# Optimization experiments

Hardware: AMD Instinct MI355X
Metric: run time of the kernel (lower is better)

Reference implementation:

```python
import jax, jax.numpy as jnp
import numpy as np

B, T, N_STOCKS = 256, 250, 500
HIDDEN, N_LAYERS = 512, 2
LB, UB = 0.0, 0.1
N_ITER = 30  # rebalance fixed-point iterations; extra iters are exact no-ops once converged


def setup_inputs() -> dict:
    key = jax.random.key(0)
    ks = jax.random.split(key, 16)
    s = 1.0 / np.sqrt(HIDDEN)  # torch GRU init scale
    inp = {"x": jax.random.normal(ks[0], (B, T, N_STOCKS), jnp.float32)}
    in_dims = [N_STOCKS, HIDDEN]
    for l in range(N_LAYERS):
        inp[f"w_ih_l{l}"] = jax.random.uniform(ks[1 + 4 * l], (3 * HIDDEN, in_dims[l]), jnp.float32, -s, s)
        inp[f"w_hh_l{l}"] = jax.random.uniform(ks[2 + 4 * l], (3 * HIDDEN, HIDDEN), jnp.float32, -s, s)
        inp[f"b_ih_l{l}"] = jax.random.uniform(ks[3 + 4 * l], (3 * HIDDEN,), jnp.float32, -s, s)
        inp[f"b_hh_l{l}"] = jax.random.uniform(ks[4 + 4 * l], (3 * HIDDEN,), jnp.float32, -s, s)
    inp["fc_w"] = jax.random.uniform(ks[9], (N_STOCKS, HIDDEN), jnp.float32, -s, s)
    inp["fc_b"] = jax.random.uniform(ks[10], (N_STOCKS,), jnp.float32, -s, s)
    return inp


def gru_layer(x, w_ih, w_hh, b_ih, b_hh):
    # x: [B, T, D] -> hidden sequence [B, T, H]; torch gate order: r, z, n
    gi = jnp.einsum('btd,gd->btg', x, w_ih) + b_ih  # precompute input gates [B, T, 3H]

    def cell(h, gi_t):
        gh = h @ w_hh.T + b_hh
        i_r, i_z, i_n = jnp.split(gi_t, 3, axis=-1)
        h_r, h_z, h_n = jnp.split(gh, 3, axis=-1)
        r = jax.nn.sigmoid(i_r + h_r)
        z = jax.nn.sigmoid(i_z + h_z)
        n = jnp.tanh(i_n + r * h_n)
        h_new = (1.0 - z) * n + z * h
        return h_new, h_new

    h0 = jnp.zeros((x.shape[0], HIDDEN), x.dtype)
    _, hs = jax.lax.scan(cell, h0, jnp.swapaxes(gi, 0, 1))  # scan over time
    return jnp.swapaxes(hs, 0, 1)


def rebalance(w):
    # Batched capped-simplex redistribution: clamp to [LB, UB], then push the
    # clipped mass onto non-capped entries proportionally; repeat to fixed point.
    def body(w, _):
        wc = jnp.clip(w, LB, UB)
        leftover = jnp.sum(w - wc, axis=-1, keepdims=True)
        nom = jnp.where(wc != UB, wc, 0.0)
        w_new = wc + leftover * nom / jnp.sum(nom, axis=-1, keepdims=True)
        return w_new, None

    w, _ = jax.lax.scan(body, w, None, length=N_ITER)
    return w


def reference(x, w_ih_l0, w_hh_l0, b_ih_l0, b_hh_l0,
              w_ih_l1, w_hh_l1, b_ih_l1, b_hh_l1, fc_w, fc_b):
    h = gru_layer(x, w_ih_l0, w_hh_l0, b_ih_l0, b_hh_l0)
    h = gru_layer(h, w_ih_l1, w_hh_l1, b_ih_l1, b_hh_l1)
    h_t = h[:, -1, :]                      # last timestep [B, H]
    logit = h_t @ fc_w.T + fc_b            # dropout is identity at inference
    logit = jax.nn.silu(logit)             # swish
    w = jax.nn.softmax(logit, axis=-1)
    return rebalance(w)
```

## Files before the change

kernel.cpp:

```cpp
#include <hip/hip_runtime.h>
#include <math.h>

typedef __attribute__((ext_vector_type(8))) short short8;
typedef __attribute__((ext_vector_type(4))) float floatx4;
typedef unsigned short ushort_t;
typedef unsigned int uint32;
typedef unsigned long long u64;

#define BB 256
#define TT 250
#define NS 500
#define HH 512
#define NBLK 256
#define TBLK 256
#define PL_USH 131072u
#define CH_USH 8192u
#define WHI_USH 32768
#define SMEMB 131072

__device__ __forceinline__ ushort_t f2bf(float f) {
    uint32 u = __float_as_uint(f);
    u += 0x7fffu + ((u >> 16) & 1u);
    return (ushort_t)(u >> 16);
}
__device__ __forceinline__ float bf2f(ushort_t h) { return __uint_as_float(((uint32)h) << 16); }
__device__ __forceinline__ float sigm(float x) { return 1.f / (1.f + expf(-x)); }
__device__ __forceinline__ floatx4 mfma16(short8 a, short8 b, floatx4 c) {
    return __builtin_amdgcn_mfma_f32_16x16x32_bf16(a, b, c, 0, 0, 0);
}
__device__ __forceinline__ u64 pack4(const ushort_t* a) {
    return (u64)a[0] | ((u64)a[1] << 16) | ((u64)a[2] << 32) | ((u64)a[3] << 48);
}
__device__ __forceinline__ void st_agent_u32(ushort_t* p, uint32 v) {
    __hip_atomic_store((uint32*)p, v, __ATOMIC_RELAXED, __HIP_MEMORY_SCOPE_AGENT);
}
__device__ __forceinline__ void st_agent_u64(ushort_t* p, u64 v) {
    __hip_atomic_store((u64*)p, v, __ATOMIC_RELAXED, __HIP_MEMORY_SCOPE_AGENT);
}

__device__ __forceinline__ void dbar(unsigned* flags, unsigned phase, int bid) {
    __syncthreads();
    if (threadIdx.x == 0)
        __hip_atomic_store(flags + ((size_t)bid << 4), phase,
                           __ATOMIC_RELAXED, __HIP_MEMORY_SCOPE_AGENT);
    unsigned* sp = flags + ((size_t)threadIdx.x << 4);
    while (__hip_atomic_load(sp, __ATOMIC_RELAXED, __HIP_MEMORY_SCOPE_AGENT) < phase)
        __builtin_amdgcn_s_sleep(2);
    __syncthreads();
}

__device__ __forceinline__ float block_max4(float v, float* scr) {
#pragma unroll
    for (int off = 32; off; off >>= 1) v = fmaxf(v, __shfl_down(v, off, 64));
    if ((threadIdx.x & 63) == 0) scr[threadIdx.x >> 6] = v;
    __syncthreads();
    if (threadIdx.x == 0)
        scr[8] = fmaxf(fmaxf(scr[0], scr[1]), fmaxf(scr[2], scr[3]));
    __syncthreads();
    float r = scr[8];
    __syncthreads();
    return r;
}
__device__ __forceinline__ float2 block_sum2_4(float a, float b, float* scr) {
#pragma unroll
    for (int off = 32; off; off >>= 1) {
        a += __shfl_down(a, off, 64);
        b += __shfl_down(b, off, 64);
    }
    if ((threadIdx.x & 63) == 0) { int w = threadIdx.x >> 6; scr[w] = a; scr[4 + w] = b; }
    __syncthreads();
    if (threadIdx.x == 0) {
        scr[8] = scr[0] + scr[1] + scr[2] + scr[3];
        scr[9] = scr[4] + scr[5] + scr[6] + scr[7];
    }
    __syncthreads();
    float2 r = make_float2(scr[8], scr[9]);
    __syncthreads();
    return r;
}

__device__ __forceinline__ void gemm_both(const ushort_t* __restrict__ gp,
                                          const ushort_t* __restrict__ hp,
                                          const ushort_t* whiS, const ushort_t* wloS,
                                          floatx4 (&aGI)[2][2], floatx4 (&aGH)[2][2]) {
    short8 Bh0[12], Bh1[12], Bl0[12], Bl1[12];
    const ushort_t* gpl = gp + PL_USH;
    const ushort_t* hpl = hp + PL_USH;

#define ISSUE(pc) do {                                                                    \
        const ushort_t* _ph = ((pc) < 16) ? (gp + (size_t)(pc) * CH_USH)                  \
                                          : (hp + (size_t)((pc) - 16) * CH_USH);          \
        const ushort_t* _pl = ((pc) < 16) ? (gpl + (size_t)(pc) * CH_USH)                 \
                                          : (hpl + (size_t)((pc) - 16) * CH_USH);         \
        asm volatile("global_load_dwordx4 %0, %1, off sc0 sc1"                            \
                     : "=v"(Bh0[(pc) % 12]) : "v"(_ph));                                  \
        asm volatile("global_load_dwordx4 %0, %1, off offset:1024 sc0 sc1"                \
                     : "=v"(Bh1[(pc) % 12]) : "v"(_ph));                                  \
        asm volatile("global_load_dwordx4 %0, %1, off sc0 sc1"                            \
                     : "=v"(Bl0[(pc) % 12]) : "v"(_pl));                                  \
        asm volatile("global_load_dwordx4 %0, %1, off offset:1024 sc0 sc1"                \
                     : "=v"(Bl1[(pc) % 12]) : "v"(_pl));                                  \
    } while (0)

    ISSUE(0); ISSUE(1); ISSUE(2); ISSUE(3); ISSUE(4); ISSUE(5);
    ISSUE(6); ISSUE(7); ISSUE(8); ISSUE(9); ISSUE(10);

    short8 w0h = *(const short8*)(whiS);
    short8 w1h = *(const short8*)(whiS + 512);
    short8 w0l = *(const short8*)(wloS);
    short8 w1l = *(const short8*)(wloS + 512);

#define GSTEP(c, N) do {                                                                  \
        if ((c) + 11 < 32) ISSUE((c) + 11);                                               \
        short8 n0h, n1h, n0l, n1l;                                                        \
        if ((c) + 1 < 32) {                                                               \
            const size_t _w = (size_t)(((c) + 1) * 2) * 512;                              \
            n0h = *(const short8*)(whiS + _w);                                            \
            n1h = *(const short8*)(whiS + _w + 512);                                      \
            n0l = *(const short8*)(wloS + _w);                                            \
            n1l = *(const short8*)(wloS + _w + 512);                                      \
        }                                                                                 \
        asm volatile("s_waitcnt vmcnt(" #N ")" ::: "memory");                             \
        __builtin_amdgcn_sched_barrier(0);                                                \
        const int _cs = (c) % 12;                                                         \
        floatx4 (&A)[2][2] = ((c) < 16) ? aGI : aGH;                                      \
        A[0][0] = mfma16(w0h, Bh0[_cs], A[0][0]);                                         \
        A[0][1] = mfma16(w0h, Bh1[_cs], A[0][1]);                                         \
        A[1][0] = mfma16(w1h, Bh0[_cs], A[1][0]);                                         \
        A[1][1] = mfma16(w1h, Bh1[_cs], A[1][1]);                                         \
        A[0][0] = mfma16(w0h, Bl0[_cs], A[0][0]);                                         \
        A[0][1] = mfma16(w0h, Bl1[_cs], A[0][1]);                                         \
        A[1][0] = mfma16(w1h, Bl0[_cs], A[1][0]);                                         \
        A[1][1] = mfma16(w1h, Bl1[_cs], A[1][1]);                                         \
        A[0][0] = mfma16(w0l, Bh0[_cs], A[0][0]);                                         \
        A[0][1] = mfma16(w0l, Bh1[_cs], A[0][1]);                                         \
        A[1][0] = mfma16(w1l, Bh0[_cs], A[1][0]);                                         \
        A[1][1] = mfma16(w1l, Bh1[_cs], A[1][1]);                                         \
        if ((c) + 1 < 32) { w0h = n0h; w1h = n1h; w0l = n0l; w1l = n1l; }                 \
    } while (0)

    GSTEP(0, 44);  GSTEP(1, 44);  GSTEP(2, 44);  GSTEP(3, 44);  GSTEP(4, 44);
    GSTEP(5, 44);  GSTEP(6, 44);  GSTEP(7, 44);  GSTEP(8, 44);  GSTEP(9, 44);
    GSTEP(10, 44); GSTEP(11, 44); GSTEP(12, 44); GSTEP(13, 44); GSTEP(14, 44);
    GSTEP(15, 44); GSTEP(16, 44); GSTEP(17, 44); GSTEP(18, 44); GSTEP(19, 44);
    GSTEP(20, 44); GSTEP(21, 40); GSTEP(22, 36); GSTEP(23, 32); GSTEP(24, 28);
    GSTEP(25, 24); GSTEP(26, 20); GSTEP(27, 16); GSTEP(28, 12); GSTEP(29, 8);
    GSTEP(30, 4);  GSTEP(31, 0);
#undef GSTEP
#undef ISSUE
}

__global__ void __launch_bounds__(TBLK, 1)
gru_main(const float* __restrict__ x,
         const float* __restrict__ wih0, const float* __restrict__ whh0,
         const float* __restrict__ bi0,  const float* __restrict__ bh0,
         const float* __restrict__ wih1, const float* __restrict__ whh1,
         const float* __restrict__ bi1,  const float* __restrict__ bh1,
         const float* __restrict__ fcb,  const float* __restrict__ fcT,
         ushort_t* xpack, ushort_t* h0pack, ushort_t* h1pack,
         unsigned* flags,
         float* __restrict__ out)
{
    extern __shared__ char smem_raw[];
    ushort_t* whi = (ushort_t*)smem_raw;
    ushort_t* wlo = whi + WHI_USH;

    const int bid = blockIdx.x, tid = threadIdx.x;
    const int L  = bid >> 7;
    const int UG = (bid >> 1) & 63;
    const int CT = bid & 1;
    const int wid = tid >> 6, lane = tid & 63;

    {
        const float* Wgi = L ? wih1 : wih0;
        const float* Wgh = L ? whh1 : whh0;
        const int Kgi = L ? HH : NS;
        for (int idx = tid; idx < 32768; idx += TBLK) {
            const int j = idx & 7, ln = (idx >> 3) & 63, rc = idx >> 9;
            const int c = rc >> 1, rt = rc & 1;
            const int m = ln & 15, qq = ln >> 4;
            const int lr = rt * 16 + m;
            const int g = lr >> 3, u = lr & 7;
            float v = 0.f;
            if (g < 3) {
                if (c < 16) {
                    const int k = c * 32 + qq * 8 + j;
                    if (k < Kgi) v = Wgi[(size_t)(g * HH + UG * 8 + u) * Kgi + k];
                } else {
                    const int k = (c - 16) * 32 + qq * 8 + j;
                    v = Wgh[(size_t)(g * HH + UG * 8 + u) * HH + k];
                }
            }
            const ushort_t hb = f2bf(v);
            whi[idx] = hb;
            wlo[idx] = f2bf(v - bf2f(hb));
        }
    }

    const int ub = ((lane >> 4) & 1) * 4;
    float biR[4], biZ[4], biN[4], bhR[4], bhZ[4], bhN[4];
    {
        const float* bi = L ? bi1 : bi0;
        const float* bh = L ? bh1 : bh0;
#pragma unroll
        for (int p = 0; p < 4; ++p) {
            const int ugl = UG * 8 + ub + p;
            biR[p] = bi[ugl]; biZ[p] = bi[HH + ugl]; biN[p] = bi[2 * HH + ugl];
            bhR[p] = bh[ugl]; bhZ[p] = bh[HH + ugl]; bhN[p] = bh[2 * HH + ugl];
        }
    }
    float hreg[2][4] = {{0.f, 0.f, 0.f, 0.f}, {0.f, 0.f, 0.f, 0.f}};
    const int chW = UG >> 2, qqW = UG & 3;
    __syncthreads();

    const ushort_t* whiS = whi + (size_t)lane * 8;
    const ushort_t* wloS = wlo + (size_t)lane * 8;
    const size_t apoff = ((size_t)(CT * 8 + wid * 2) * 64 + lane) * 8;

    unsigned phase = 0;
    for (int s = 0; s <= TT; ++s) {
        const bool active = L ? (s >= 1) : (s < TT);
        if (active) {
            const ushort_t *gisrc, *ghsrc;
            if (L == 0) {
                gisrc = xpack + (size_t)(s & 1) * 2 * PL_USH;
                ghsrc = h0pack + (size_t)((s - 1) & 1) * 2 * PL_USH;
            } else {
                gisrc = h0pack + (size_t)((s - 1) & 1) * 2 * PL_USH;
                ghsrc = h1pack + (size_t)(s & 1) * 2 * PL_USH;
            }
            floatx4 z4 = {0.f, 0.f, 0.f, 0.f};
            floatx4 aGI[2][2], aGH[2][2];
#pragma unroll
            for (int i = 0; i < 2; ++i) { aGI[i][0] = z4; aGI[i][1] = z4; aGH[i][0] = z4; aGH[i][1] = z4; }
            gemm_both(gisrc + apoff, ghsrc + apoff, whiS, wloS, aGI, aGH);

            float4 xv0, xv1;
            const bool doX = (s <= TT - 2) && (bid * TBLK + tid < 16384);
            int xko = 0, xb = 0;
            if (doX) {
                const int gx = bid * TBLK + tid;
                xko = gx & 63; xb = gx >> 6;
                const float* xs = x + ((size_t)xb * TT + (s + 1)) * NS + xko * 8;
                if (xko < 62) { xv0 = *(const float4*)(xs); xv1 = *(const float4*)(xs + 4); }
                else {
                    float tmp[8];
#pragma unroll
                    for (int j = 0; j < 8; ++j) {
                        const int k = xko * 8 + j;
                        tmp[j] = (k < NS) ? xs[j] : 0.f;
                    }
                    xv0 = make_float4(tmp[0], tmp[1], tmp[2], tmp[3]);
                    xv1 = make_float4(tmp[4], tmp[5], tmp[6], tmp[7]);
                }
            }

            float zGI[2][4], zGH[2][4];
#pragma unroll
            for (int t = 0; t < 2; ++t)
#pragma unroll
                for (int r = 0; r < 4; ++r) {
                    zGI[t][r] = __shfl_xor(aGI[0][t][r], 32, 64);
                    zGH[t][r] = __shfl_xor(aGH[0][t][r], 32, 64);
                }
            ushort_t* pk = L ? h1pack + (size_t)((s - 1) & 1) * 2 * PL_USH
                             : h0pack + (size_t)(s & 1) * 2 * PL_USH;
            if (lane < 32) {
#pragma unroll
                for (int t = 0; t < 2; ++t) {
                    ushort_t hi4[4], lo4[4];
#pragma unroll
                    for (int r = 0; r < 4; ++r) {
                        const float gir = aGI[0][t][r], ghr = aGH[0][t][r];
                        const float giz = zGI[t][r],    ghz = zGH[t][r];
                        const float gin = aGI[1][t][r], ghn = aGH[1][t][r];
                        const float rr = sigm(gir + biR[r] + ghr + bhR[r]);
                        const float zz = sigm(giz + biZ[r] + ghz + bhZ[r]);
                        const float nn = tanhf(gin + biN[r] + rr * (ghn + bhN[r]));
                        const float hv = (1.f - zz) * nn + zz * hreg[t][r];
                        hreg[t][r] = hv;
                        hi4[r] = f2bf(hv);
                        lo4[r] = f2bf(hv - bf2f(hi4[r]));
                    }
                    const int b = CT * 128 + wid * 32 + t * 16 + (lane & 15);
                    const size_t o8 = ((size_t)(chW * 16 + (b >> 4)) * 64 + qqW * 16 + (b & 15)) * 8 + ub;
                    st_agent_u32(pk + o8,     (uint32)hi4[0] | ((uint32)hi4[1] << 16));
                    st_agent_u32(pk + o8 + 2, (uint32)hi4[2] | ((uint32)hi4[3] << 16));
                    st_agent_u32(pk + PL_USH + o8,     (uint32)lo4[0] | ((uint32)lo4[1] << 16));
                    st_agent_u32(pk + PL_USH + o8 + 2, (uint32)lo4[2] | ((uint32)lo4[3] << 16));
                }
            }

            if (doX) {
                ushort_t hi8[8], lo8[8];
                float vv[8] = {xv0.x, xv0.y, xv0.z, xv0.w, xv1.x, xv1.y, xv1.z, xv1.w};
#pragma unroll
                for (int j = 0; j < 8; ++j) {
                    hi8[j] = f2bf(vv[j]);
                    lo8[j] = f2bf(vv[j] - bf2f(hi8[j]));
                }
                ushort_t* xp = xpack + (size_t)((s + 1) & 1) * 2 * PL_USH;
                const size_t o = ((size_t)((xko >> 2) * 16 + (xb >> 4)) * 64 + (xko & 3) * 16 + (xb & 15)) * 8;
                st_agent_u64(xp + o, pack4(hi8));
                st_agent_u64(xp + o + 4, pack4(hi8 + 4));
                st_agent_u64(xp + PL_USH + o, pack4(lo8));
                st_agent_u64(xp + PL_USH + o + 4, pack4(lo8 + 4));
            }
        } else if ((s <= TT - 2) && (bid * TBLK + tid < 16384)) {
            const int gx = bid * TBLK + tid;
            const int xko = gx & 63, xb = gx >> 6;
            const float* xs = x + ((size_t)xb * TT + (s + 1)) * NS + xko * 8;
            ushort_t hi8[8], lo8[8];
#pragma unroll
            for (int j = 0; j < 8; ++j) {
                const int k = xko * 8 + j;
                const float v = (k < NS) ? xs[j] : 0.f;
                hi8[j] = f2bf(v);
                lo8[j] = f2bf(v - bf2f(hi8[j]));
            }
            ushort_t* xp = xpack + (size_t)((s + 1) & 1) * 2 * PL_USH;
            const size_t o = ((size_t)((xko >> 2) * 16 + (xb >> 4)) * 64 + (xko & 3) * 16 + (xb & 15)) * 8;
            st_agent_u64(xp + o, pack4(hi8));
            st_agent_u64(xp + o + 4, pack4(hi8 + 4));
            st_agent_u64(xp + PL_USH + o, pack4(lo8));
            st_agent_u64(xp + PL_USH + o + 4, pack4(lo8 + 4));
        }
        ++phase;
        dbar(flags, phase, bid);
    }

    {
        const int b = bid;
        float* sh = (float*)smem_raw;
        float* scr = sh + 576;
        const ushort_t* pk = h1pack + (size_t)1 * 2 * PL_USH;
        for (int u = tid; u < HH; u += TBLK) {
            const int uo = u >> 3, j = u & 7;
            const size_t o = ((size_t)((uo >> 2) * 16 + (b >> 4)) * 64 + (uo & 3) * 16 + (b & 15)) * 8 + j;
            sh[u] = bf2f(pk[o]) + bf2f(pk[PL_USH + o]);
        }
        __syncthreads();

        const int o1 = tid;
        const bool v2 = (tid + 256) < NS;
        const int o2 = v2 ? (tid + 256) : (NS - 1);
        float a0 = fcb[o1], a1 = fcb[o2];
        for (int k = 0; k < HH; ++k) {
            const float hv = sh[k];
            const float* fr = fcT + (size_t)k * NS;
            a0 = fmaf(hv, fr[o1], a0);
            a1 = fmaf(hv, fr[o2], a1);
        }
        float l0 = a0 * sigm(a0);
        float l1 = a1 * sigm(a1);
        float mx = block_max4(fmaxf(l0, v2 ? l1 : -3.4e38f), scr);
        float e0 = expf(l0 - mx);
        float e1 = v2 ? expf(l1 - mx) : 0.f;
        float2 s2 = block_sum2_4(e0 + e1, 0.f, scr);
        float w0 = e0 / s2.x, w1 = e1 / s2.x;
        for (int it = 0; it < 30; ++it) {
            float c0v = fminf(fmaxf(w0, 0.f), 0.1f);
            float c1v = fminf(fmaxf(w1, 0.f), 0.1f);
            float lv = (w0 - c0v) + (w1 - c1v);
            float n0 = (c0v != 0.1f) ? c0v : 0.f;
            float n1 = (v2 && c1v != 0.1f) ? c1v : 0.f;
            float2 rs = block_sum2_4(lv, n0 + n1, scr);
            float inv = rs.x / rs.y;
            w0 = c0v + inv * n0;
            w1 = c1v + inv * n1;
        }
        out[(size_t)b * NS + o1] = w0;
        if (v2) out[(size_t)b * NS + tid + 256] = w1;
    }
}

__global__ void pack_x0(const float* __restrict__ x, ushort_t* __restrict__ xpack) {
    const int t = blockIdx.x * 256 + threadIdx.x;
    const int ko = t & 63, b = t >> 6;
    const float* xs = x + (size_t)b * TT * NS;
    ushort_t hi8[8], lo8[8];
#pragma unroll
    for (int j = 0; j < 8; ++j) {
        const int k = ko * 8 + j;
        const float v = (k < NS) ? xs[k] : 0.f;
        hi8[j] = f2bf(v);
        lo8[j] = f2bf(v - bf2f(hi8[j]));
    }
    const size_t o = ((size_t)((ko >> 2) * 16 + (b >> 4)) * 64 + (ko & 3) * 16 + (b & 15)) * 8;
    *(uint4*)(xpack + o) = *(uint4*)hi8;
    *(uint4*)(xpack + PL_USH + o) = *(uint4*)lo8;
}

__global__ void transpose_k(const float* __restrict__ src, float* __restrict__ dst,
                            int G, int K) {
    int idx = blockIdx.x * 256 + threadIdx.x;
    if (idx >= G * K) return;
    int k = idx / G, g = idx - k * G;
    dst[idx] = src[(size_t)g * K + k];
}

extern "C" void kernel_launch(void* const* d_in, const int* in_sizes, int n_in,
                              void* d_out, int out_size, void* d_ws, size_t ws_size,
                              hipStream_t stream) {
    const float* x    = (const float*)d_in[0];
    const float* wih0 = (const float*)d_in[1];
    const float* whh0 = (const float*)d_in[2];
    const float* bih0 = (const float*)d_in[3];
    const float* bhh0 = (const float*)d_in[4];
    const float* wih1 = (const float*)d_in[5];
    const float* whh1 = (const float*)d_in[6];
    const float* bih1 = (const float*)d_in[7];
    const float* bhh1 = (const float*)d_in[8];
    const float* fcw  = (const float*)d_in[9];
    const float* fcb  = (const float*)d_in[10];
    float* outp = (float*)d_out;

    char* ws = (char*)d_ws;
    unsigned* flags  = (unsigned*)ws;
    ushort_t* h0pack = (ushort_t*)(ws + 196608);
    ushort_t* h1pack = (ushort_t*)(ws + 196608 + 1048576);
    ushort_t* xpack  = (ushort_t*)(ws + 196608 + 2097152);
    float*    fcT    = (float*)(ws + 196608 + 3145728);

    hipMemsetAsync(ws, 0, 196608 + 2097152, stream);
    pack_x0<<<64, 256, 0, stream>>>(x, xpack);
    {
        int nel = NS * HH;
        transpose_k<<<(nel + 255) / 256, 256, 0, stream>>>(fcw, fcT, NS, HH);
    }

    hipFuncSetAttribute((const void*)gru_main,
                        hipFuncAttributeMaxDynamicSharedMemorySize, SMEMB);

    void* args[] = {(void*)&x,
                    (void*)&wih0, (void*)&whh0, (void*)&bih0, (void*)&bhh0,
                    (void*)&wih1, (void*)&whh1, (void*)&bih1, (void*)&bhh1,
                    (void*)&fcb, (void*)&fcT,
                    (void*)&xpack, (void*)&h0pack, (void*)&h1pack,
                    (void*)&flags, (void*)&outp};
    hipError_t e = hipLaunchCooperativeKernel((const void*)gru_main, dim3(NBLK), dim3(TBLK),
                                              args, SMEMB, stream);
    if (e != hipSuccess) {
        gru_main<<<dim3(NBLK), dim3(TBLK), SMEMB, stream>>>(
            x, wih0, whh0, bih0, bhh0, wih1, whh1, bih1, bhh1,
            fcb, fcT, xpack, h0pack, h1pack, flags, outp);
    }
}
```

Measured before the change: 3.342 ms.

## Use hierarchical per-XCD grid barrier with explicit fences instead of coherent stores

Replaces the flat all-blocks grid barrier with a two-level barrier. Each XCD elects a leader block that waits for its members, issues a release fence, and exchanges completion flags with the other XCD leaders before an acquire fence. Member blocks then poll a single per-XCD flag. Because the fences now provide visibility, hidden-state and x stores become plain wide stores, and the GEMM loads drop the sc1 bit. The intent is to cut polling traffic and per-store coherence cost on every timestep. The risk is memory-ordering bugs, since correctness now depends on the fences covering L2 writeback and invalidation across XCDs.

Measured after the change: 5.774 ms. 1.73x slower.

```diff
diff --git a/kernel.cpp b/kernel.cpp
--- a/kernel.cpp
+++ b/kernel.cpp
@@ -31,22 +31,56 @@
 __device__ __forceinline__ u64 pack4(const ushort_t* a) {
     return (u64)a[0] | ((u64)a[1] << 16) | ((u64)a[2] << 32) | ((u64)a[3] << 48);
 }
-__device__ __forceinline__ void st_agent_u32(ushort_t* p, uint32 v) {
-    __hip_atomic_store((uint32*)p, v, __ATOMIC_RELAXED, __HIP_MEMORY_SCOPE_AGENT);
-}
-__device__ __forceinline__ void st_agent_u64(ushort_t* p, u64 v) {
-    __hip_atomic_store((u64*)p, v, __ATOMIC_RELAXED, __HIP_MEMORY_SCOPE_AGENT);
-}
-
-__device__ __forceinline__ void dbar(unsigned* flags, unsigned phase, int bid) {
-    __syncthreads();
-    if (threadIdx.x == 0)
-        __hip_atomic_store(flags + ((size_t)bid << 4), phase,
-                           __ATOMIC_RELAXED, __HIP_MEMORY_SCOPE_AGENT);
+__device__ __forceinline__ void st_flag(unsigned* p, unsigned v) {
+    __hip_atomic_store(p, v, __ATOMIC_RELAXED, __HIP_MEMORY_SCOPE_AGENT);
+}
+__device__ __forceinline__ unsigned ld_flag(const unsigned* p) {
+    return __hip_atomic_load(p, __ATOMIC_RELAXED, __HIP_MEMORY_SCOPE_AGENT);
+}
+
+
+__device__ __forceinline__ void dbar_flat(unsigned* flags, unsigned phase, int bid) {
+    __syncthreads();
+    if (threadIdx.x == 0) st_flag(flags + ((size_t)bid << 4), phase);
     unsigned* sp = flags + ((size_t)threadIdx.x << 4);
-    while (__hip_atomic_load(sp, __ATOMIC_RELAXED, __HIP_MEMORY_SCOPE_AGENT) < phase)
-        __builtin_amdgcn_s_sleep(2);
-    __syncthreads();
+    while (ld_flag(sp) < phase) __builtin_amdgcn_s_sleep(2);
+    __syncthreads();
+}
+
+__device__ __forceinline__ void dbar2(unsigned* flags, unsigned phase, int bid,
+                                      int myxcd, bool isLead, unsigned cnt,
+                                      unsigned mymem, bool wact) {
+    unsigned* wbdone  = flags + 4096;
+    unsigned* invdone = flags + 8192;
+    __syncthreads();
+    if (threadIdx.x == 0) st_flag(flags + ((size_t)bid << 4), phase);
+    if (isLead) {
+        if (threadIdx.x < cnt) {
+            unsigned* sp = flags + ((size_t)mymem << 4);
+            while (ld_flag(sp) < phase) __builtin_amdgcn_s_sleep(2);
+        }
+        __syncthreads();
+        if (threadIdx.x == 0) {
+            __builtin_amdgcn_fence(__ATOMIC_RELEASE, "agent");
+            st_flag(wbdone + ((size_t)myxcd << 4), phase);
+        }
+        if (threadIdx.x < 8 && wact) {
+            unsigned* sp = wbdone + ((size_t)threadIdx.x << 4);
+            while (ld_flag(sp) < phase) __builtin_amdgcn_s_sleep(2);
+        }
+        __syncthreads();
+        if (threadIdx.x == 0) {
+            __builtin_amdgcn_fence(__ATOMIC_ACQUIRE, "agent");
+            st_flag(invdone + ((size_t)myxcd << 4), phase);
+        }
+        __syncthreads();
+    } else {
+        if (threadIdx.x == 0) {
+            unsigned* sp = invdone + ((size_t)myxcd << 4);
+            while (ld_flag(sp) < phase) __builtin_amdgcn_s_sleep(2);
+        }
+        __syncthreads();
+    }
 }
 
 __device__ __forceinline__ float block_max4(float v, float* scr) {
@@ -92,13 +126,13 @@
                                           : (hp + (size_t)((pc) - 16) * CH_USH);          \
         const ushort_t* _pl = ((pc) < 16) ? (gpl + (size_t)(pc) * CH_USH)                 \
                                           : (hpl + (size_t)((pc) - 16) * CH_USH);         \
-        asm volatile("global_load_dwordx4 %0, %1, off sc0 sc1"                            \
+        asm volatile("global_load_dwordx4 %0, %1, off sc0"                                \
                      : "=v"(Bh0[(pc) % 12]) : "v"(_ph));                                  \
-        asm volatile("global_load_dwordx4 %0, %1, off offset:1024 sc0 sc1"                \
+        asm volatile("global_load_dwordx4 %0, %1, off offset:1024 sc0"                    \
                      : "=v"(Bh1[(pc) % 12]) : "v"(_ph));                                  \
-        asm volatile("global_load_dwordx4 %0, %1, off sc0 sc1"                            \
+        asm volatile("global_load_dwordx4 %0, %1, off sc0"                                \
                      : "=v"(Bl0[(pc) % 12]) : "v"(_pl));                                  \
-        asm volatile("global_load_dwordx4 %0, %1, off offset:1024 sc0 sc1"                \
+        asm volatile("global_load_dwordx4 %0, %1, off offset:1024 sc0"                    \
                      : "=v"(Bl1[(pc) % 12]) : "v"(_pl));                                  \
     } while (0)
 
@@ -162,6 +196,7 @@
          float* __restrict__ out)
 {
     extern __shared__ char smem_raw[];
+    __shared__ unsigned s_bc;
     ushort_t* whi = (ushort_t*)smem_raw;
     ushort_t* wlo = whi + WHI_USH;
 
@@ -197,6 +232,32 @@
         }
     }
 
+    int myxcd;
+    asm volatile("s_getreg_b32 %0, hwreg(HW_REG_XCC_ID)" : "=s"(myxcd));
+    myxcd &= 7;
+    unsigned* xcnt = flags + 12288;
+    unsigned* xmem = flags + 16384;
+    if (tid == 0) {
+        unsigned slot = atomicAdd(xcnt + ((size_t)myxcd << 4), 1u);
+        if (slot < 64) st_flag(xmem + myxcd * 64 + slot, (unsigned)bid);
+        asm volatile("s_waitcnt vmcnt(0)" ::: "memory");
+        s_bc = slot;
+    }
+    __syncthreads();
+    const bool isLead = (s_bc == 0);
+    __syncthreads();
+
+    dbar_flat(flags, 1, bid);
+
+    unsigned cnt = 0, mymem = 0;
+    bool wact = false;
+    if (isLead) {
+        cnt = ld_flag(xcnt + ((size_t)myxcd << 4));
+        if (cnt > 64) cnt = 64;
+        if (tid < cnt) mymem = ld_flag(xmem + myxcd * 64 + tid);
+        if (tid < 8) wact = (ld_flag(xcnt + ((size_t)tid << 4)) > 0);
+    }
+
     const int ub = ((lane >> 4) & 1) * 4;
     float biR[4], biZ[4], biN[4], bhR[4], bhZ[4], bhN[4];
     {
@@ -217,8 +278,8 @@
     const ushort_t* wloS = wlo + (size_t)lane * 8;
     const size_t apoff = ((size_t)(CT * 8 + wid * 2) * 64 + lane) * 8;
 
-    unsigned phase = 0;
     for (int s = 0; s <= TT; ++s) {
+        const unsigned phase = (unsigned)s + 2;
         const bool active = L ? (s >= 1) : (s < TT);
         if (active) {
             const ushort_t *gisrc, *ghsrc;
@@ -284,10 +345,8 @@
                     }
                     const int b = CT * 128 + wid * 32 + t * 16 + (lane & 15);
                     const size_t o8 = ((size_t)(chW * 16 + (b >> 4)) * 64 + qqW * 16 + (b & 15)) * 8 + ub;
-                    st_agent_u32(pk + o8,     (uint32)hi4[0] | ((uint32)hi4[1] << 16));
-                    st_agent_u32(pk + o8 + 2, (uint32)hi4[2] | ((uint32)hi4[3] << 16));
-                    st_agent_u32(pk + PL_USH + o8,     (uint32)lo4[0] | ((uint32)lo4[1] << 16));
-                    st_agent_u32(pk + PL_USH + o8 + 2, (uint32)lo4[2] | ((uint32)lo4[3] << 16));
+                    *(u64*)(pk + o8) = pack4(hi4);
+                    *(u64*)(pk + PL_USH + o8) = pack4(lo4);
                 }
             }
 
@@ -301,10 +360,8 @@
                 }
                 ushort_t* xp = xpack + (size_t)((s + 1) & 1) * 2 * PL_USH;
                 const size_t o = ((size_t)((xko >> 2) * 16 + (xb >> 4)) * 64 + (xko & 3) * 16 + (xb & 15)) * 8;
-                st_agent_u64(xp + o, pack4(hi8));
-                st_agent_u64(xp + o + 4, pack4(hi8 + 4));
-                st_agent_u64(xp + PL_USH + o, pack4(lo8));
-                st_agent_u64(xp + PL_USH + o + 4, pack4(lo8 + 4));
+                *(uint4*)(xp + o) = *(uint4*)hi8;
+                *(uint4*)(xp + PL_USH + o) = *(uint4*)lo8;
             }
         } else if ((s <= TT - 2) && (bid * TBLK + tid < 16384)) {
             const int gx = bid * TBLK + tid;
@@ -320,13 +377,10 @@
             }
             ushort_t* xp = xpack + (size_t)((s + 1) & 1) * 2 * PL_USH;
             const size_t o = ((size_t)((xko >> 2) * 16 + (xb >> 4)) * 64 + (xko & 3) * 16 + (xb & 15)) * 8;
-            st_agent_u64(xp + o, pack4(hi8));
-            st_agent_u64(xp + o + 4, pack4(hi8 + 4));
-            st_agent_u64(xp + PL_USH + o, pack4(lo8));
-            st_agent_u64(xp + PL_USH + o + 4, pack4(lo8 + 4));
-        }
-        ++phase;
-        dbar(flags, phase, bid);
+            *(uint4*)(xp + o) = *(uint4*)hi8;
+            *(uint4*)(xp + PL_USH + o) = *(uint4*)lo8;
+        }
+        dbar2(flags, phase, bid, myxcd, isLead, cnt, mymem, wact);
     }
 
     {
```

## Double block threads to 512 so each wave computes one 16-column batch tile

Applied to the files above, without the earlier changes.

The persistent GRU kernel now runs 512 threads per block instead of 256. Each wave handles a single 16-wide batch tile instead of two, which halves per-wave accumulators, B-operand loads and MFMA count, and adjusts the load-wait counts to match. Hidden-state stores become single 64-bit atomic stores, and the final FC/softmax/rebalance stage is rewritten so each thread handles one output. This trades more waves per CU, and so more latency hiding per recurrent step, for higher register and LDS pressure and more barrier participants.

New measurement: 3.327 ms. Within noise of the previous version (-0.5%).

```diff
diff --git a/kernel.cpp b/kernel.cpp
--- a/kernel.cpp
+++ b/kernel.cpp
@@ -12,7 +12,7 @@
 #define NS 500
 #define HH 512
 #define NBLK 256
-#define TBLK 256
+#define TBLK 512
 #define PL_USH 131072u
 #define CH_USH 8192u
 #define WHI_USH 32768
@@ -31,11 +31,13 @@
 __device__ __forceinline__ u64 pack4(const ushort_t* a) {
     return (u64)a[0] | ((u64)a[1] << 16) | ((u64)a[2] << 32) | ((u64)a[3] << 48);
 }
-__device__ __forceinline__ void st_agent_u32(ushort_t* p, uint32 v) {
-    __hip_atomic_store((uint32*)p, v, __ATOMIC_RELAXED, __HIP_MEMORY_SCOPE_AGENT);
-}
 __device__ __forceinline__ void st_agent_u64(ushort_t* p, u64 v) {
     __hip_atomic_store((u64*)p, v, __ATOMIC_RELAXED, __HIP_MEMORY_SCOPE_AGENT);
+}
+__device__ __forceinline__ void st_agent_u64x(uint4* p, uint4 v) {
+    u64* q = (u64*)p;
+    __hip_atomic_store(q,     (u64)v.x | ((u64)v.y << 32), __ATOMIC_RELAXED, __HIP_MEMORY_SCOPE_AGENT);
+    __hip_atomic_store(q + 1, (u64)v.z | ((u64)v.w << 32), __ATOMIC_RELAXED, __HIP_MEMORY_SCOPE_AGENT);
 }
 
 __device__ __forceinline__ void dbar(unsigned* flags, unsigned phase, int bid) {
@@ -43,38 +45,46 @@
     if (threadIdx.x == 0)
         __hip_atomic_store(flags + ((size_t)bid << 4), phase,
                            __ATOMIC_RELAXED, __HIP_MEMORY_SCOPE_AGENT);
-    unsigned* sp = flags + ((size_t)threadIdx.x << 4);
-    while (__hip_atomic_load(sp, __ATOMIC_RELAXED, __HIP_MEMORY_SCOPE_AGENT) < phase)
-        __builtin_amdgcn_s_sleep(2);
-    __syncthreads();
-}
-
-__device__ __forceinline__ float block_max4(float v, float* scr) {
+    if (threadIdx.x < NBLK) {
+        unsigned* sp = flags + ((size_t)threadIdx.x << 4);
+        while (__hip_atomic_load(sp, __ATOMIC_RELAXED, __HIP_MEMORY_SCOPE_AGENT) < phase)
+            __builtin_amdgcn_s_sleep(2);
+    }
+    __syncthreads();
+}
+
+__device__ __forceinline__ float block_max8(float v, float* scr) {
 #pragma unroll
     for (int off = 32; off; off >>= 1) v = fmaxf(v, __shfl_down(v, off, 64));
     if ((threadIdx.x & 63) == 0) scr[threadIdx.x >> 6] = v;
     __syncthreads();
-    if (threadIdx.x == 0)
-        scr[8] = fmaxf(fmaxf(scr[0], scr[1]), fmaxf(scr[2], scr[3]));
-    __syncthreads();
-    float r = scr[8];
+    if (threadIdx.x == 0) {
+        float m = scr[0];
+#pragma unroll
+        for (int w = 1; w < 8; ++w) m = fmaxf(m, scr[w]);
+        scr[16] = m;
+    }
+    __syncthreads();
+    float r = scr[16];
     __syncthreads();
     return r;
 }
-__device__ __forceinline__ float2 block_sum2_4(float a, float b, float* scr) {
+__device__ __forceinline__ float2 block_sum2_8(float a, float b, float* scr) {
 #pragma unroll
     for (int off = 32; off; off >>= 1) {
         a += __shfl_down(a, off, 64);
         b += __shfl_down(b, off, 64);
     }
-    if ((threadIdx.x & 63) == 0) { int w = threadIdx.x >> 6; scr[w] = a; scr[4 + w] = b; }
+    if ((threadIdx.x & 63) == 0) { int w = threadIdx.x >> 6; scr[w] = a; scr[8 + w] = b; }
     __syncthreads();
     if (threadIdx.x == 0) {
-        scr[8] = scr[0] + scr[1] + scr[2] + scr[3];
-        scr[9] = scr[4] + scr[5] + scr[6] + scr[7];
-    }
-    __syncthreads();
-    float2 r = make_float2(scr[8], scr[9]);
+        float sa = 0.f, sb = 0.f;
+#pragma unroll
+        for (int w = 0; w < 8; ++w) { sa += scr[w]; sb += scr[8 + w]; }
+        scr[16] = sa; scr[17] = sb;
+    }
+    __syncthreads();
+    float2 r = make_float2(scr[16], scr[17]);
     __syncthreads();
     return r;
 }
@@ -82,8 +92,8 @@
 __device__ __forceinline__ void gemm_both(const ushort_t* __restrict__ gp,
                                           const ushort_t* __restrict__ hp,
                                           const ushort_t* whiS, const ushort_t* wloS,
-                                          floatx4 (&aGI)[2][2], floatx4 (&aGH)[2][2]) {
-    short8 Bh0[12], Bh1[12], Bl0[12], Bl1[12];
+                                          floatx4 (&aGI)[2], floatx4 (&aGH)[2]) {
+    short8 Bh[12], Bl[12];
     const ushort_t* gpl = gp + PL_USH;
     const ushort_t* hpl = hp + PL_USH;
 
@@ -93,13 +103,9 @@
         const ushort_t* _pl = ((pc) < 16) ? (gpl + (size_t)(pc) * CH_USH)                 \
                                           : (hpl + (size_t)((pc) - 16) * CH_USH);         \
         asm volatile("global_load_dwordx4 %0, %1, off sc0 sc1"                            \
-                     : "=v"(Bh0[(pc) % 12]) : "v"(_ph));                                  \
-        asm volatile("global_load_dwordx4 %0, %1, off offset:1024 sc0 sc1"                \
-                     : "=v"(Bh1[(pc) % 12]) : "v"(_ph));                                  \
+                     : "=v"(Bh[(pc) % 12]) : "v"(_ph));                                   \
         asm volatile("global_load_dwordx4 %0, %1, off sc0 sc1"                            \
-                     : "=v"(Bl0[(pc) % 12]) : "v"(_pl));                                  \
-        asm volatile("global_load_dwordx4 %0, %1, off offset:1024 sc0 sc1"                \
-                     : "=v"(Bl1[(pc) % 12]) : "v"(_pl));                                  \
+                     : "=v"(Bl[(pc) % 12]) : "v"(_pl));                                   \
     } while (0)
 
     ISSUE(0); ISSUE(1); ISSUE(2); ISSUE(3); ISSUE(4); ISSUE(5);
@@ -123,34 +129,28 @@
         asm volatile("s_waitcnt vmcnt(" #N ")" ::: "memory");                             \
         __builtin_amdgcn_sched_barrier(0);                                                \
         const int _cs = (c) % 12;                                                         \
-        floatx4 (&A)[2][2] = ((c) < 16) ? aGI : aGH;                                      \
-        A[0][0] = mfma16(w0h, Bh0[_cs], A[0][0]);                                         \
-        A[0][1] = mfma16(w0h, Bh1[_cs], A[0][1]);                                         \
-        A[1][0] = mfma16(w1h, Bh0[_cs], A[1][0]);                                         \
-        A[1][1] = mfma16(w1h, Bh1[_cs], A[1][1]);                                         \
-        A[0][0] = mfma16(w0h, Bl0[_cs], A[0][0]);                                         \
-        A[0][1] = mfma16(w0h, Bl1[_cs], A[0][1]);                                         \
-        A[1][0] = mfma16(w1h, Bl0[_cs], A[1][0]);                                         \
-        A[1][1] = mfma16(w1h, Bl1[_cs], A[1][1]);                                         \
-        A[0][0] = mfma16(w0l, Bh0[_cs], A[0][0]);                                         \
-        A[0][1] = mfma16(w0l, Bh1[_cs], A[0][1]);                                         \
-        A[1][0] = mfma16(w1l, Bh0[_cs], A[1][0]);                                         \
-        A[1][1] = mfma16(w1l, Bh1[_cs], A[1][1]);                                         \
+        floatx4 (&A)[2] = ((c) < 16) ? aGI : aGH;                                         \
+        A[0] = mfma16(w0h, Bh[_cs], A[0]);                                                \
+        A[1] = mfma16(w1h, Bh[_cs], A[1]);                                                \
+        A[0] = mfma16(w0h, Bl[_cs], A[0]);                                                \
+        A[1] = mfma16(w1h, Bl[_cs], A[1]);                                                \
+        A[0] = mfma16(w0l, Bh[_cs], A[0]);                                                \
+        A[1] = mfma16(w1l, Bh[_cs], A[1]);                                                \
         if ((c) + 1 < 32) { w0h = n0h; w1h = n1h; w0l = n0l; w1l = n1l; }                 \
     } while (0)
 
-    GSTEP(0, 44);  GSTEP(1, 44);  GSTEP(2, 44);  GSTEP(3, 44);  GSTEP(4, 44);
-    GSTEP(5, 44);  GSTEP(6, 44);  GSTEP(7, 44);  GSTEP(8, 44);  GSTEP(9, 44);
-    GSTEP(10, 44); GSTEP(11, 44); GSTEP(12, 44); GSTEP(13, 44); GSTEP(14, 44);
-    GSTEP(15, 44); GSTEP(16, 44); GSTEP(17, 44); GSTEP(18, 44); GSTEP(19, 44);
-    GSTEP(20, 44); GSTEP(21, 40); GSTEP(22, 36); GSTEP(23, 32); GSTEP(24, 28);
-    GSTEP(25, 24); GSTEP(26, 20); GSTEP(27, 16); GSTEP(28, 12); GSTEP(29, 8);
-    GSTEP(30, 4);  GSTEP(31, 0);
+    GSTEP(0, 22);  GSTEP(1, 22);  GSTEP(2, 22);  GSTEP(3, 22);  GSTEP(4, 22);
+    GSTEP(5, 22);  GSTEP(6, 22);  GSTEP(7, 22);  GSTEP(8, 22);  GSTEP(9, 22);
+    GSTEP(10, 22); GSTEP(11, 22); GSTEP(12, 22); GSTEP(13, 22); GSTEP(14, 22);
+    GSTEP(15, 22); GSTEP(16, 22); GSTEP(17, 22); GSTEP(18, 22); GSTEP(19, 22);
+    GSTEP(20, 22); GSTEP(21, 20); GSTEP(22, 18); GSTEP(23, 16); GSTEP(24, 14);
+    GSTEP(25, 12); GSTEP(26, 10); GSTEP(27, 8);  GSTEP(28, 6);  GSTEP(29, 4);
+    GSTEP(30, 2);  GSTEP(31, 0);
 #undef GSTEP
 #undef ISSUE
 }
 
-__global__ void __launch_bounds__(TBLK, 1)
+__global__ void __launch_bounds__(TBLK, 2)
 gru_main(const float* __restrict__ x,
          const float* __restrict__ wih0, const float* __restrict__ whh0,
          const float* __restrict__ bi0,  const float* __restrict__ bh0,
@@ -209,16 +209,16 @@
             bhR[p] = bh[ugl]; bhZ[p] = bh[HH + ugl]; bhN[p] = bh[2 * HH + ugl];
         }
     }
-    float hreg[2][4] = {{0.f, 0.f, 0.f, 0.f}, {0.f, 0.f, 0.f, 0.f}};
+    float hreg[4] = {0.f, 0.f, 0.f, 0.f};
     const int chW = UG >> 2, qqW = UG & 3;
     __syncthreads();
 
     const ushort_t* whiS = whi + (size_t)lane * 8;
     const ushort_t* wloS = wlo + (size_t)lane * 8;
-    const size_t apoff = ((size_t)(CT * 8 + wid * 2) * 64 + lane) * 8;
-
-    unsigned phase = 0;
+    const size_t apoff = ((size_t)(CT * 8 + wid) * 64 + lane) * 8;
+
     for (int s = 0; s <= TT; ++s) {
+        const unsigned phase = (unsigned)s + 1;
         const bool active = L ? (s >= 1) : (s < TT);
         if (active) {
             const ushort_t *gisrc, *ghsrc;
@@ -230,9 +230,8 @@
                 ghsrc = h1pack + (size_t)(s & 1) * 2 * PL_USH;
             }
             floatx4 z4 = {0.f, 0.f, 0.f, 0.f};
-            floatx4 aGI[2][2], aGH[2][2];
-#pragma unroll
-            for (int i = 0; i < 2; ++i) { aGI[i][0] = z4; aGI[i][1] = z4; aGH[i][0] = z4; aGH[i][1] = z4; }
+            floatx4 aGI[2], aGH[2];
+            aGI[0] = z4; aGI[1] = z4; aGH[0] = z4; aGH[1] = z4;
             gemm_both(gisrc + apoff, ghsrc + apoff, whiS, wloS, aGI, aGH);
 
             float4 xv0, xv1;
@@ -255,40 +254,33 @@
                 }
             }
 
-            float zGI[2][4], zGH[2][4];
-#pragma unroll
-            for (int t = 0; t < 2; ++t)
-#pragma unroll
-                for (int r = 0; r < 4; ++r) {
-                    zGI[t][r] = __shfl_xor(aGI[0][t][r], 32, 64);
-                    zGH[t][r] = __shfl_xor(aGH[0][t][r], 32, 64);
-                }
+            float zGI[4], zGH[4];
+#pragma unroll
+            for (int r = 0; r < 4; ++r) {
+                zGI[r] = __shfl_xor(aGI[0][r], 32, 64);
+                zGH[r] = __shfl_xor(aGH[0][r], 32, 64);
+            }
             ushort_t* pk = L ? h1pack + (size_t)((s - 1) & 1) * 2 * PL_USH
                              : h0pack + (size_t)(s & 1) * 2 * PL_USH;
             if (lane < 32) {
-#pragma unroll
-                for (int t = 0; t < 2; ++t) {
-                    ushort_t hi4[4], lo4[4];
-#pragma unroll
-                    for (int r = 0; r < 4; ++r) {
-                        const float gir = aGI[0][t][r], ghr = aGH[0][t][r];
-                        const float giz = zGI[t][r],    ghz = zGH[t][r];
-                        const float gin = aGI[1][t][r], ghn = aGH[1][t][r];
-                        const float rr = sigm(gir + biR[r] + ghr + bhR[r]);
-                        const float zz = sigm(giz + biZ[r] + ghz + bhZ[r]);
-                        const float nn = tanhf(gin + biN[r] + rr * (ghn + bhN[r]));
-                        const float hv = (1.f - zz) * nn + zz * hreg[t][r];
-                        hreg[t][r] = hv;
-                        hi4[r] = f2bf(hv);
-                        lo4[r] = f2bf(hv - bf2f(hi4[r]));
-                    }
-                    const int b = CT * 128 + wid * 32 + t * 16 + (lane & 15);
-                    const size_t o8 = ((size_t)(chW * 16 + (b >> 4)) * 64 + qqW * 16 + (b & 15)) * 8 + ub;
-                    st_agent_u32(pk + o8,     (uint32)hi4[0] | ((uint32)hi4[1] << 16));
-                    st_agent_u32(pk + o8 + 2, (uint32)hi4[2] | ((uint32)hi4[3] << 16));
-                    st_agent_u32(pk + PL_USH + o8,     (uint32)lo4[0] | ((uint32)lo4[1] << 16));
-                    st_agent_u32(pk + PL_USH + o8 + 2, (uint32)lo4[2] | ((uint32)lo4[3] << 16));
+                ushort_t hi4[4], lo4[4];
+#pragma unroll
+                for (int r = 0; r < 4; ++r) {
+                    const float gir = aGI[0][r], ghr = aGH[0][r];
+                    const float giz = zGI[r],    ghz = zGH[r];
+                    const float gin = aGI[1][r], ghn = aGH[1][r];
+                    const float rr = sigm(gir + biR[r] + ghr + bhR[r]);
+                    const float zz = sigm(giz + biZ[r] + ghz + bhZ[r]);
+                    const float nn = tanhf(gin + biN[r] + rr * (ghn + bhN[r]));
+                    const float hv = (1.f - zz) * nn + zz * hreg[r];
+                    hreg[r] = hv;
+                    hi4[r] = f2bf(hv);
+                    lo4[r] = f2bf(hv - bf2f(hi4[r]));
                 }
+                const int b = CT * 128 + wid * 16 + (lane & 15);
+                const size_t o8 = ((size_t)(chW * 16 + (b >> 4)) * 64 + qqW * 16 + (b & 15)) * 8 + ub;
+                st_agent_u64(pk + o8, pack4(hi4));
+                st_agent_u64(pk + PL_USH + o8, pack4(lo4));
             }
 
             if (doX) {
@@ -325,52 +317,40 @@
             st_agent_u64(xp + PL_USH + o, pack4(lo8));
             st_agent_u64(xp + PL_USH + o + 4, pack4(lo8 + 4));
         }
-        ++phase;
         dbar(flags, phase, bid);
     }
 
     {
         const int b = bid;
         float* sh = (float*)smem_raw;
-        float* scr = sh + 576;
+        float* scr = sh + 512;
         const ushort_t* pk = h1pack + (size_t)1 * 2 * PL_USH;
-        for (int u = tid; u < HH; u += TBLK) {
+        {
+            const int u = tid;
             const int uo = u >> 3, j = u & 7;
             const size_t o = ((size_t)((uo >> 2) * 16 + (b >> 4)) * 64 + (uo & 3) * 16 + (b & 15)) * 8 + j;
             sh[u] = bf2f(pk[o]) + bf2f(pk[PL_USH + o]);
         }
         __syncthreads();
 
-        const int o1 = tid;
-        const bool v2 = (tid + 256) < NS;
-        const int o2 = v2 ? (tid + 256) : (NS - 1);
-        float a0 = fcb[o1], a1 = fcb[o2];
-        for (int k = 0; k < HH; ++k) {
-            const float hv = sh[k];
-            const float* fr = fcT + (size_t)k * NS;
-            a0 = fmaf(hv, fr[o1], a0);
-            a1 = fmaf(hv, fr[o2], a1);
-        }
+        const bool valid = tid < NS;
+        const int o1 = valid ? tid : 0;
+        float a0 = fcb[o1];
+        for (int k = 0; k < HH; ++k)
+            a0 = fmaf(sh[k], fcT[(size_t)k * NS + o1], a0);
         float l0 = a0 * sigm(a0);
-        float l1 = a1 * sigm(a1);
-        float mx = block_max4(fmaxf(l0, v2 ? l1 : -3.4e38f), scr);
-        float e0 = expf(l0 - mx);
-        float e1 = v2 ? expf(l1 - mx) : 0.f;
-        float2 s2 = block_sum2_4(e0 + e1, 0.f, scr);
-        float w0 = e0 / s2.x, w1 = e1 / s2.x;
+        float mx = block_max8(valid ? l0 : -3.4e38f, scr);
+        float e0 = valid ? expf(l0 - mx) : 0.f;
+        float2 s2 = block_sum2_8(e0, 0.f, scr);
+        float w0 = e0 / s2.x;
         for (int it = 0; it < 30; ++it) {
             float c0v = fminf(fmaxf(w0, 0.f), 0.1f);
-            float c1v = fminf(fmaxf(w1, 0.f), 0.1f);
-            float lv = (w0 - c0v) + (w1 - c1v);
+            float lv = w0 - c0v;
             float n0 = (c0v != 0.1f) ? c0v : 0.f;
-            float n1 = (v2 && c1v != 0.1f) ? c1v : 0.f;
-            float2 rs = block_sum2_4(lv, n0 + n1, scr);
-            float inv = rs.x / rs.y;
-            w0 = c0v + inv * n0;
-            w1 = c1v + inv * n1;
+            float2 rs = block_sum2_8(lv, n0, scr);
+            w0 = c0v + rs.x / rs.y * n0;
         }
-        out[(size_t)b * NS + o1] = w0;
-        if (v2) out[(size_t)b * NS + tid + 256] = w1;
+        if (valid) out[(size_t)b * NS + tid] = w0;
     }
 }
 
```
